# Kernel tuning notes

Measured on AMD Instinct MI355X. Metric: run time of the kernel, lower is better.

Reference implementation:

```python
import jax, jax.numpy as jnp
import numpy as np

DEPTH = 6; HEADS = 6; DIM = 384; HD = DIM // HEADS
WS = 14; WINDOW_BLOCKS = (0, 1, 3, 4)
IMG = 512; PATCH = 16; GRID = IMG // PATCH        # 32x32 token grid
PRE_GRID = 14                                      # 224 // 16 pretrain grid
SCALE = HD ** -0.5


def layer_norm(x, w, b, eps=1e-5):
    u = x.mean(-1, keepdims=True)
    s = ((x - u) ** 2).mean(-1, keepdims=True)
    return (x - u) / jnp.sqrt(s + eps) * w + b


def get_rel_pos(size, rel_pos):
    # q_size == k_size here; relative coords in [0, 2*size-2]
    coords = jnp.arange(size)[:, None] - jnp.arange(size)[None, :] + (size - 1)
    return rel_pos[coords]  # (size, size, HD)


def attention(x, qkv_w, qkv_b, proj_w, proj_b, rel_h, rel_w):
    B, H, W, C = x.shape
    N = H * W
    qkv = (x.reshape(B, N, C) @ qkv_w.T + qkv_b).reshape(B, N, 3, HEADS, HD)
    qkv = jnp.moveaxis(qkv, 2, 0).transpose(0, 1, 3, 2, 4)  # (3,B,h,N,d)
    q, k, v = qkv[0], qkv[1], qkv[2]
    attn = jnp.einsum('bhqd,bhkd->bhqk', q * SCALE, k)
    # decomposed relative position bias (ViTDet add_decomposed_rel_pos)
    Rh = get_rel_pos(H, rel_h)  # (H,H,d)
    Rw = get_rel_pos(W, rel_w)  # (W,W,d)
    rq = q.reshape(B, HEADS, H, W, HD)
    bias_h = jnp.einsum('bnhwc,hkc->bnhwk', rq, Rh)  # (B,h,H,W,H)
    bias_w = jnp.einsum('bnhwc,wkc->bnhwk', rq, Rw)  # (B,h,H,W,W)
    attn = (attn.reshape(B, HEADS, H, W, H, W)
            + bias_h[..., :, None] + bias_w[..., None, :]).reshape(B, HEADS, N, N)
    attn = jax.nn.softmax(attn, axis=-1)
    out = jnp.einsum('bhqk,bhkd->bhqd', attn, v)
    out = out.transpose(0, 2, 1, 3).reshape(B, H, W, C)
    return out @ proj_w.T + proj_b


def window_partition(x, ws):
    B, H, W, C = x.shape
    pad_h = (ws - H % ws) % ws
    pad_w = (ws - W % ws) % ws
    x = jnp.pad(x, ((0, 0), (0, pad_h), (0, pad_w), (0, 0)))
    Hp, Wp = H + pad_h, W + pad_w
    x = x.reshape(B, Hp // ws, ws, Wp // ws, ws, C)
    x = x.transpose(0, 1, 3, 2, 4, 5).reshape(-1, ws, ws, C)
    return x, Hp, Wp


def window_unpartition(win, ws, Hp, Wp, H, W):
    B = win.shape[0] // ((Hp // ws) * (Wp // ws))
    x = win.reshape(B, Hp // ws, Wp // ws, ws, ws, -1)
    x = x.transpose(0, 1, 3, 2, 4, 5).reshape(B, Hp, Wp, -1)
    return x[:, :H, :W]


def block(x, p, windowed):
    shortcut = x
    x = layer_norm(x, p['n1w'], p['n1b'])
    if windowed:
        H, W = x.shape[1], x.shape[2]
        x, Hp, Wp = window_partition(x, WS)
    x = attention(x, p['qw'], p['qb'], p['pw'], p['pb'], p['rh'], p['rw'])
    if windowed:
        x = window_unpartition(x, WS, Hp, Wp, H, W)
    x = shortcut + x
    h = layer_norm(x, p['n2w'], p['n2b'])
    h = jax.nn.gelu(h @ p['f1w'].T + p['f1b'], approximate=False)
    return x + h @ p['f2w'].T + p['f2b']


def vit_forward(x, patch_w, patch_b, pos_embed, norm1_w, norm1_b, qkv_w, qkv_b,
                proj_w, proj_b, norm2_w, norm2_b, fc1_w, fc1_b, fc2_w, fc2_b,
                rel_pos_h, rel_pos_w):
    y = jax.lax.conv_general_dilated(
        x, patch_w, (PATCH, PATCH), 'VALID',
        dimension_numbers=('NCHW', 'OIHW', 'NCHW'))
    y = y.transpose(0, 2, 3, 1) + patch_b  # (B, GRID, GRID, DIM)
    # abs pos embed: bicubic resize from pretrain 14x14 grid to 32x32
    pos = pos_embed.reshape(1, PRE_GRID, PRE_GRID, DIM)
    pos = jax.image.resize(pos, (1, GRID, GRID, DIM), 'bicubic')
    y = y + pos
    for i in range(DEPTH):
        windowed = i in WINDOW_BLOCKS
        L = 2 * WS - 1 if windowed else 2 * GRID - 1
        p = dict(n1w=norm1_w[i], n1b=norm1_b[i], qw=qkv_w[i], qb=qkv_b[i],
                 pw=proj_w[i], pb=proj_b[i], rh=rel_pos_h[i, :L], rw=rel_pos_w[i, :L],
                 n2w=norm2_w[i], n2b=norm2_b[i], f1w=fc1_w[i], f1b=fc1_b[i],
                 f2w=fc2_w[i], f2b=fc2_b[i])
        y = block(y, p, windowed)
    return y.transpose(0, 3, 1, 2)  # (B, DIM, GRID, GRID) 'last_feat'


def setup_inputs() -> dict:
    key = jax.random.key(0)
    ks = jax.random.split(key, 10)
    B = 4
    std = 0.02
    f32 = jnp.float32
    return {
        'x': jax.random.normal(ks[0], (B, 3, IMG, IMG), f32),
        'patch_w': jax.random.normal(ks[1], (DIM, 3, PATCH, PATCH), f32) * 0.05,
        'patch_b': jnp.zeros((DIM,), f32),
        'pos_embed': jax.random.normal(ks[2], (1, PRE_GRID * PRE_GRID, DIM), f32) * std,
        'norm1_w': jnp.ones((DEPTH, DIM), f32),
        'norm1_b': jnp.zeros((DEPTH, DIM), f32),
        'qkv_w': jax.random.normal(ks[3], (DEPTH, 3 * DIM, DIM), f32) * std,
        'qkv_b': jnp.zeros((DEPTH, 3 * DIM), f32),
        'proj_w': jax.random.normal(ks[4], (DEPTH, DIM, DIM), f32) * std,
        'proj_b': jnp.zeros((DEPTH, DIM), f32),
        'norm2_w': jnp.ones((DEPTH, DIM), f32),
        'norm2_b': jnp.zeros((DEPTH, DIM), f32),
        'fc1_w': jax.random.normal(ks[5], (DEPTH, 4 * DIM, DIM), f32) * std,
        'fc1_b': jnp.zeros((DEPTH, 4 * DIM), f32),
        'fc2_w': jax.random.normal(ks[6], (DEPTH, DIM, 4 * DIM), f32) * std,
        'fc2_b': jnp.zeros((DEPTH, DIM), f32),
        'rel_pos_h': jax.random.normal(ks[7], (DEPTH, 2 * GRID - 1, HD), f32) * std,
        'rel_pos_w': jax.random.normal(ks[8], (DEPTH, 2 * GRID - 1, HD), f32) * std,
    }


def reference(x, patch_w, patch_b, pos_embed, norm1_w, norm1_b, qkv_w, qkv_b,
              proj_w, proj_b, norm2_w, norm2_b, fc1_w, fc1_b, fc2_w, fc2_b,
              rel_pos_h, rel_pos_w):
    return vit_forward(x, patch_w, patch_b, pos_embed, norm1_w, norm1_b, qkv_w, qkv_b,
                       proj_w, proj_b, norm2_w, norm2_b, fc1_w, fc1_b, fc2_w, fc2_b,
                       rel_pos_h, rel_pos_w)
```

## Files before the change

### kernel.cpp

```cpp
#include <hip/hip_runtime.h>
#include <hip/hip_bf16.h>
#include <math.h>

#define B_SZ 4
#define DIM 384
#define HEADS 6
#define HD 64
#define NTOK 4096
#define WS 14
#define NWIN 36
#define WTOK 196

typedef unsigned short u16;
typedef __bf16 bf16_t;
typedef bf16_t bf16x8 __attribute__((ext_vector_type(8)));
typedef float f32x4 __attribute__((ext_vector_type(4)));

__device__ __forceinline__ float bf2f(unsigned u) { return __uint_as_float(u << 16); }
__device__ __forceinline__ u16 f2bf(float f) {
    unsigned u = __float_as_uint(f);
    unsigned r = (u + 0x7fffu + ((u >> 16) & 1u)) >> 16;
    return (u16)r;
}
__device__ __forceinline__ unsigned pk2bf(float a, float b) {
    __hip_bfloat162 h = __float22bfloat162_rn(make_float2(a, b));
    unsigned r; __builtin_memcpy(&r, &h, 4); return r;
}

__device__ __forceinline__ void ldsload16(const u16* g, u16* l) {
    __builtin_amdgcn_global_load_lds(
        (const __attribute__((address_space(1))) unsigned int*)g,
        (__attribute__((address_space(3))) unsigned int*)l, 16, 0, 0);
}

__device__ __forceinline__ int swz(int r) { return (r ^ (r >> 2)) & 3; }

__device__ inline float cubic_keys(float x) {
    x = fabsf(x);
    if (x <= 1.f) return ((1.5f * x - 2.5f) * x) * x + 1.f;
    if (x < 2.f)  return ((-0.5f * x + 2.5f) * x - 4.f) * x + 2.f;
    return 0.f;
}

__global__ __launch_bounds__(256) void setup_kernel(
        const float* __restrict__ p0, const float* __restrict__ p1,
        const float* __restrict__ p2, const float* __restrict__ p3,
        const float* __restrict__ p4, const float* __restrict__ p5,
        u16* __restrict__ wb, const float* __restrict__ pe,
        float* __restrict__ posr, const float* __restrict__ x,
        u16* __restrict__ col) {
    int i = (blockIdx.x * 256 + threadIdx.x) * 4;
    if (i < 10918656) {
        const float* s; int off;
        if      (i <   294912) { s = p0; off = 0; }
        else if (i <  2949120) { s = p1; off = 294912; }
        else if (i <  3833856) { s = p2; off = 2949120; }
        else if (i <  7372800) { s = p3; off = 3833856; }
        else if (i < 10911744) { s = p4; off = 7372800; }
        else                   { s = p5; off = 10911744; }
        float4 v = *(const float4*)(s + (i - off));
        u16 o[4] = { f2bf(v.x), f2bf(v.y), f2bf(v.z), f2bf(v.w) };
        *(uint2*)(wb + i) = *(const uint2*)o;
        return;
    }
    i -= 10918656;
    if (i < 393216) {
        int c = i % 384;
        int g = i / 384;
        int gy = g / 32, gx = g % 32;
        float wy[14], wx[14];
        float sy = (gy + 0.5f) * (14.f / 32.f) - 0.5f;
        float sx = (gx + 0.5f) * (14.f / 32.f) - 0.5f;
        float toty = 0.f, totx = 0.f;
        #pragma unroll
        for (int k = 0; k < 14; ++k) {
            wy[k] = cubic_keys(sy - (float)k); toty += wy[k];
            wx[k] = cubic_keys(sx - (float)k); totx += wx[k];
        }
        float4 acc = {0.f, 0.f, 0.f, 0.f};
        #pragma unroll 1
        for (int iy = 0; iy < 14; ++iy) {
            if (wy[iy] == 0.f) continue;
            float4 row = {0.f, 0.f, 0.f, 0.f};
            for (int ix = 0; ix < 14; ++ix) {
                if (wx[ix] == 0.f) continue;
                float4 pv = *(const float4*)(pe + (iy * 14 + ix) * 384 + c);
                row.x += wx[ix] * pv.x; row.y += wx[ix] * pv.y;
                row.z += wx[ix] * pv.z; row.w += wx[ix] * pv.w;
            }
            acc.x += wy[iy] * row.x; acc.y += wy[iy] * row.y;
            acc.z += wy[iy] * row.z; acc.w += wy[iy] * row.w;
        }
        float inv = 1.f / (toty * totx);
        acc.x *= inv; acc.y *= inv; acc.z *= inv; acc.w *= inv;
        *(float4*)(posr + i) = acc;
        return;
    }
    i -= 393216;
    if (i < 3145728) {
        int kk = i % 768;
        int p  = i / 768;
        int b  = p / 1024;
        int ph = (p % 1024) / 32;
        int pw = p % 32;
        int c = kk / 256;
        int r = kk % 256;
        int ii = r / 16, j = r % 16;
        float4 v = *(const float4*)(x + (size_t)b * 3 * 512 * 512 +
                                    (size_t)c * 512 * 512 +
                                    (size_t)(ph * 16 + ii) * 512 + (pw * 16 + j));
        u16 o[4] = { f2bf(v.x), f2bf(v.y), f2bf(v.z), f2bf(v.w) };
        *(uint2*)(col + i) = *(const uint2*)o;
    }
}

__global__ __launch_bounds__(64) void epi_ln_kernel(const float* __restrict__ P,
        const float* __restrict__ bias, const float* __restrict__ posr,
        float* __restrict__ y, int addy, int nsk,
        const float* __restrict__ lw, const float* __restrict__ lb,
        u16* __restrict__ lnout, float* __restrict__ outT)
{
    int tok = blockIdx.x, t = threadIdx.x;
    size_t base = (size_t)tok * 384;
    float v[6];
    float s = 0.f;
    #pragma unroll
    for (int i = 0; i < 6; ++i) {
        int c = t + 64 * i;
        float val = bias[c];
        #pragma unroll 1
        for (int sk = 0; sk < nsk; ++sk)
            val += P[(size_t)sk * 1572864 + base + c];
        if (posr) val += posr[(size_t)(tok & 1023) * 384 + c];
        if (addy) val += y[base + c];
        v[i] = val; s += val;
    }
    if (outT) {
        int b = tok >> 10, g = tok & 1023;
        #pragma unroll
        for (int i = 0; i < 6; ++i) {
            int c = t + 64 * i;
            outT[((size_t)(b * 384 + c)) * 1024 + g] = v[i];
        }
        return;
    }
    #pragma unroll
    for (int i = 0; i < 6; ++i) y[base + t + 64 * i] = v[i];
    if (!lnout) return;
    #pragma unroll
    for (int off = 32; off > 0; off >>= 1) s += __shfl_xor(s, off);
    float mean = s * (1.f / 384.f);
    float vs = 0.f;
    #pragma unroll
    for (int i = 0; i < 6; ++i) { float d = v[i] - mean; vs += d * d; }
    #pragma unroll
    for (int off = 32; off > 0; off >>= 1) vs += __shfl_xor(vs, off);
    float inv = rsqrtf(vs * (1.f / 384.f) + 1e-5f);
    u16* orow = lnout + base;
    #pragma unroll
    for (int i = 0; i < 6; ++i) {
        int c = t + 64 * i;
        orow[c] = f2bf((v[i] - mean) * inv * lw[c] + lb[c]);
    }
}

__global__ __launch_bounds__(256) void mfma_gemm4(
        const u16* __restrict__ A, const u16* __restrict__ Wt,
        const float* __restrict__ bias,
        float* __restrict__ outf, u16* __restrict__ outb,
        float* __restrict__ outp,
        int M, int N, int K, int act, int ksplit)
{
    __shared__ u16 As[2][8192];
    __shared__ u16 Bs[2][4096];
    int t = threadIdx.x;
    int lane = t & 63, wave = t >> 6;
    int wm = (wave >> 1) * 64, wn = (wave & 1) * 32;
    int m0 = blockIdx.y * 128, n0 = blockIdx.x * 64;
    int ks = blockIdx.z * ksplit;

    int r0 = t >> 2,        c0 = ((t & 3) ^ swz(t >> 2)) * 8;
    int r1 = 64 + (t >> 2), c1 = ((t & 3) ^ swz(64 + (t >> 2))) * 8;
    const u16* a0 = A + (size_t)(m0 + r0) * K + c0;
    const u16* a1 = A + (size_t)(m0 + r1) * K + c1;
    const u16* b0 = Wt + (size_t)(n0 + r0) * K + c0;

    auto stage = [&](int k0, int buf) {
        ldsload16(a0 + k0,      &As[buf][wave * 512]);
        ldsload16(a1 + k0,      &As[buf][2048 + wave * 512]);
        ldsload16(b0 + k0,      &Bs[buf][wave * 512]);
        ldsload16(a0 + k0 + 32, &As[buf][4096 + wave * 512]);
        ldsload16(a1 + k0 + 32, &As[buf][6144 + wave * 512]);
        ldsload16(b0 + k0 + 32, &Bs[buf][2048 + wave * 512]);
    };

    f32x4 acc[4][2] = {};
    int row_a = wm + (lane & 15);
    int row_b = wn + (lane & 15);
    int lq = lane >> 4;
    int nchunks = ksplit / 64;

    stage(ks, 0);
    __syncthreads();

    for (int ci = 0; ci < nchunks; ++ci) {
        int p = ci & 1;
        bool pref = (ci + 1 < nchunks);
        if (pref) stage(ks + (ci + 1) * 64, 1 - p);
        #pragma unroll
        for (int hf = 0; hf < 2; ++hf) {
            bf16x8 af[4], bfr[2];
            #pragma unroll
            for (int i = 0; i < 4; ++i) {
                int r = row_a + i * 16;
                af[i] = *(const bf16x8*)&As[p][hf * 4096 + r * 32 + ((lq ^ swz(r)) * 8)];
            }
            #pragma unroll
            for (int j = 0; j < 2; ++j) {
                int r = row_b + j * 16;
                bfr[j] = *(const bf16x8*)&Bs[p][hf * 2048 + r * 32 + ((lq ^ swz(r)) * 8)];
            }
            #pragma unroll
            for (int i = 0; i < 4; ++i)
                #pragma unroll
                for (int j = 0; j < 2; ++j)
                    acc[i][j] = __builtin_amdgcn_mfma_f32_16x16x32_bf16(
                        af[i], bfr[j], acc[i][j], 0, 0, 0);
        }
        if (pref) __syncthreads();
    }

    int colq = lane & 15, rowq = (lane >> 4) * 4;
    if (outp) {
        float* pp = outp + (size_t)blockIdx.z * M * N;
        #pragma unroll
        for (int i = 0; i < 4; ++i) {
            #pragma unroll
            for (int rr = 0; rr < 4; ++rr) {
                int m = m0 + wm + i * 16 + rowq + rr;
                size_t mo = (size_t)m * N;
                #pragma unroll
                for (int j = 0; j < 2; ++j) {
                    int n = n0 + wn + j * 16 + colq;
                    pp[mo + n] = acc[i][j][rr];
                }
            }
        }
        return;
    }
    #pragma unroll
    for (int i = 0; i < 4; ++i) {
        #pragma unroll
        for (int rr = 0; rr < 4; ++rr) {
            int m = m0 + wm + i * 16 + rowq + rr;
            size_t mo = (size_t)m * N;
            #pragma unroll
            for (int j = 0; j < 2; ++j) {
                int n = n0 + wn + j * 16 + colq;
                float v = acc[i][j][rr] + bias[n];
                if (act)  v = 0.5f * v * (1.f + erff(v * 0.70710678118654752f));
                if (outf) outf[mo + n] = v;
                if (outb) outb[mo + n] = f2bf(v);
            }
        }
    }
}

template<int N, int W>
__global__ __launch_bounds__(256) void attn_mfma(const u16* __restrict__ qkv,
        const u16* __restrict__ qkb, const float* __restrict__ rh,
        const float* __restrict__ rw, u16* __restrict__ outb,
        float* __restrict__ opart, float* __restrict__ lpart)
{
    constexpr int JS = (W == 32) ? 64 : 32;
    constexpr int L  = (W == 32) ? 63 : 27;
    constexpr int CTR = W - 1;
    constexpr int KSPAN = (W == 32) ? 512 : 224;
    constexpr int NKT = KSPAN / 32;
    __shared__ u16 KV[11776];
    __shared__ u16 bhl[64 * 66];
    __shared__ u16 bwl[64 * 66];
    __shared__ u16 Qt[64 * 66];

    u16* Pb = KV + 9216;
    u16* Rt = KV;

    int t = threadIdx.x, lane = t & 63, wave = t >> 6;
    int quad = lane >> 4, l15 = lane & 15;
    int uh = blockIdx.x, qb0 = blockIdx.y * 64;
    int z = (W == 32) ? blockIdx.z : 0;
    int kstart = z * KSPAN;
    int h = uh % HEADS, u = uh / HEADS;
    size_t tbase = (size_t)u * 1024;
    int wb_ = u / 9, wr = u - wb_ * 9;
    int wy = wr / 3, wx = wr - wy * 3;

    auto tok14 = [&](int iy, int ix) -> const u16* {
        int gy = wy * WS + iy, gx = wx * WS + ix;
        if (gy < 32 && gx < 32)
            return qkv + (size_t)(wb_ * 1024 + gy * 32 + gx) * 1152;
        return qkb;
    };
    auto rowptr = [&](int lq2) -> const u16* {
        if constexpr (W == 32) {
            return qkv + (tbase + lq2) * 1152;
        } else {
            int iy = lq2 / WS, ix = lq2 - iy * WS;
            return tok14(iy, ix);
        }
    };

    {
        int q = t & 63, ch0 = (t >> 6) * 16;
        int qc = qb0 + q; if (qc >= N) qc = N - 1;
        const u16* qp = rowptr(qc) + h * 64 + ch0;
        uint4 a = *(const uint4*)qp;
        uint4 b = *(const uint4*)(qp + 8);
        u16 vals[16];
        *(uint4*)vals = a; *(uint4*)(vals + 8) = b;
        #pragma unroll
        for (int c = 0; c < 16; ++c)
            Qt[(ch0 + c) * 66 + q] = ((qb0 + q) < N) ? vals[c] : (u16)0;
    }

    #pragma unroll
    for (int table = 0; table < 2; ++table) {
        __syncthreads();
        const float* tab = table ? rw : rh;
        for (int idx = t; idx < JS * 8; idx += 256) {
            int j = idx >> 3, cc0 = (idx & 7) * 8;
            u16 tmp[8];
            if (j < L) {
                const float* src = tab + (size_t)j * 64 + cc0;
                #pragma unroll
                for (int c = 0; c < 8; ++c) tmp[c] = f2bf(src[c]);
            } else {
                #pragma unroll
                for (int c = 0; c < 8; ++c) tmp[c] = 0;
            }
            *(uint4*)&Rt[j * 72 + cc0] = *(uint4*)tmp;
        }
        __syncthreads();
        if (wave < JS / 16) {
            int jt = wave;
            bf16x8 af0 = *(const bf16x8*)&Rt[(jt * 16 + l15) * 72 + quad * 8];
            bf16x8 af1 = *(const bf16x8*)&Rt[(jt * 16 + l15) * 72 + 32 + quad * 8];
            u16* dst = table ? bwl : bhl;
            #pragma unroll
            for (int qt = 0; qt < 4; ++qt) {
                bf16x8 qf0, qf1;
                u16* p0 = (u16*)&qf0; u16* p1 = (u16*)&qf1;
                #pragma unroll
                for (int zz = 0; zz < 8; ++zz) {
                    p0[zz] = Qt[(quad * 8 + zz) * 66 + qt * 16 + l15];
                    p1[zz] = Qt[(32 + quad * 8 + zz) * 66 + qt * 16 + l15];
                }
                f32x4 acc = {};
                acc = __builtin_amdgcn_mfma_f32_16x16x32_bf16(af0, qf0, acc, 0, 0, 0);
                acc = __builtin_amdgcn_mfma_f32_16x16x32_bf16(af1, qf1, acc, 0, 0, 0);
                #pragma unroll
                for (int r = 0; r < 4; ++r)
                    dst[(qt * 16 + l15) * 66 + jt * 16 + quad * 4 + r] = f2bf(acc[r]);
            }
        }
    }
    __syncthreads();

    int skey = (wave * 64 + lane) >> 3;
    int sc8  = ((wave * 64 + lane) & 7) ^ (skey & 7);
    int vkey = t & 31, vch0 = (t >> 5) * 8;
    int siy = 0, six = 0, viy = 0, vix = 0;
    if constexpr (W != 32) {
        int k0 = kstart + skey;
        siy = k0 / WS; six = k0 - siy * WS;
        int k1 = kstart + vkey;
        viy = k1 / WS; vix = k1 - viy * WS;
    }
    auto adv = [](int& iy, int& ix) { ix += 4; iy += 2; if (ix >= WS) { ix -= WS; ++iy; } };

    {
        const u16* kp = (W == 32) ? qkv + (tbase + kstart + skey) * 1152
                                  : tok14(siy, six);
        ldsload16(kp + 384 + h * 64 + sc8 * 8, KV + wave * 512);
        const u16* vp = (W == 32) ? qkv + (tbase + kstart + vkey) * 1152
                                  : tok14(viy, vix);
        uint4 vv = *(const uint4*)(vp + 768 + h * 64 + vch0);
        u16 tmp[8]; *(uint4*)tmp = vv;
        u16* vdst = KV + 4096;
        #pragma unroll
        for (int c = 0; c < 8; ++c) vdst[(vch0 + c) * 40 + vkey] = tmp[c];
        if constexpr (W != 32) { adv(siy, six); adv(viy, vix); }
    }

    bf16x8 qf[2];
    #pragma unroll
    for (int hc = 0; hc < 2; ++hc) {
        u16* qv = (u16*)&qf[hc];
        #pragma unroll
        for (int j = 0; j < 8; ++j)
            qv[j] = Qt[(hc * 32 + quad * 8 + j) * 66 + wave * 16 + l15];
    }
    int qme = wave * 16 + l15;
    int qq = qb0 + qme; if (qq >= N) qq = N - 1;
    int qh = qq / W, qw = qq - qh * W;
    float bwreg[2][4];
    int kh_[2][4], kw_[2][4];
    #pragma unroll
    for (int kc2 = 0; kc2 < 2; ++kc2)
        #pragma unroll
        for (int r = 0; r < 4; ++r) {
            int keyl = kc2 * 16 + quad * 4 + r;
            if constexpr (W == 32) {
                bwreg[kc2][r] = bf2f(bwl[qme * 66 + (qw - keyl + CTR)]);
            } else {
                kh_[kc2][r] = keyl / WS;
                kw_[kc2][r] = keyl - kh_[kc2][r] * WS;
            }
        }

    f32x4 of[4] = {};
    float lsum = 0.f;
    __syncthreads();

    for (int kt = 0; kt < NKT; ++kt) {
        int kb = kstart + kt * 32;
        int p = kt & 1;
        const u16* ksp = KV + p * 2048;
        const u16* vtp = KV + 4096 + p * 2560;
        bool pref = (kt + 1 < NKT);
        uint4 vpref;
        if (pref) {
            const u16* kp = (W == 32) ? qkv + (tbase + kb + 32 + skey) * 1152
                                      : tok14(siy, six);
            ldsload16(kp + 384 + h * 64 + sc8 * 8, KV + (1 - p) * 2048 + wave * 512);
            const u16* vp = (W == 32) ? qkv + (tbase + kb + 32 + vkey) * 1152
                                      : tok14(viy, vix);
            vpref = *(const uint4*)(vp + 768 + h * 64 + vch0);
            if constexpr (W != 32) { adv(siy, six); adv(viy, vix); }
        }

        f32x4 st[2] = {};
        #pragma unroll
        for (int hc = 0; hc < 2; ++hc) {
            #pragma unroll
            for (int kc2 = 0; kc2 < 2; ++kc2) {
                int key = kc2 * 16 + l15;
                int c8 = hc * 4 + quad;
                int pp = key * 8 + (c8 ^ (key & 7));
                bf16x8 kf = *(const bf16x8*)&ksp[pp * 8];
                st[kc2] = __builtin_amdgcn_mfma_f32_16x16x32_bf16(
                    kf, qf[hc], st[kc2], 0, 0, 0);
            }
        }
        float bh_t = 0.f;
        if constexpr (W == 32) bh_t = bf2f(bhl[qme * 66 + (qh - (kb >> 5) + CTR)]);
        #pragma unroll
        for (int kc2 = 0; kc2 < 2; ++kc2) {
            float pv4[4];
            #pragma unroll
            for (int r = 0; r < 4; ++r) {
                int keyl = kc2 * 16 + quad * 4 + r;
                float b;
                if constexpr (W == 32) {
                    b = bh_t + bwreg[kc2][r];
                } else {
                    b = bf2f(bhl[qme * 66 + (qh - kh_[kc2][r] + CTR)]) +
                        bf2f(bwl[qme * 66 + (qw - kw_[kc2][r] + CTR)]);
                }
                float pv = __expf(fmaf(st[kc2][r], 0.125f, b));
                if (kb + keyl >= N) pv = 0.f;
                lsum += pv;
                pv4[r] = pv;
            }
            uint2 pk;
            pk.x = pk2bf(pv4[0], pv4[1]);
            pk.y = pk2bf(pv4[2], pv4[3]);
            *(uint2*)&Pb[wave * 640 + l15 * 40 + kc2 * 16 + quad * 4] = pk;
        }
        if constexpr (W != 32) {
            #pragma unroll
            for (int kc2 = 0; kc2 < 2; ++kc2)
                #pragma unroll
                for (int r = 0; r < 4; ++r) {
                    kw_[kc2][r] += 4; kh_[kc2][r] += 2;
                    if (kw_[kc2][r] >= WS) { kw_[kc2][r] -= WS; ++kh_[kc2][r]; }
                }
        }
        bf16x8 pf = *(const bf16x8*)&Pb[wave * 640 + l15 * 40 + quad * 8];
        #pragma unroll
        for (int ca = 0; ca < 4; ++ca) {
            bf16x8 vf = *(const bf16x8*)&vtp[(ca * 16 + l15) * 40 + quad * 8];
            of[ca] = __builtin_amdgcn_mfma_f32_16x16x32_bf16(
                vf, pf, of[ca], 0, 0, 0);
        }

        if (pref) {
            u16 tmp[8]; *(uint4*)tmp = vpref;
            u16* vdst = KV + 4096 + (1 - p) * 2560;
            #pragma unroll
            for (int c = 0; c < 8; ++c) vdst[(vch0 + c) * 40 + vkey] = tmp[c];
            __syncthreads();
        }
    }

    lsum += __shfl_xor(lsum, 16);
    lsum += __shfl_xor(lsum, 32);
    int q = qb0 + qme;
    if constexpr (W == 32) {
        size_t ridx = (size_t)z * 24576 + (size_t)uh * 1024 + q;
        float* op = opart + ridx * 64;
        #pragma unroll
        for (int ca = 0; ca < 4; ++ca)
            *(float4*)&op[ca * 16 + quad * 4] = (float4){of[ca][0], of[ca][1],
                                                         of[ca][2], of[ca][3]};
        if (quad == 0) lpart[ridx] = lsum;
    } else {
        float inv = 1.f / lsum;
        if (q < N) {
            int iy = q / WS, ix = q - iy * WS;
            int gy = wy * WS + iy, gx = wx * WS + ix;
            if (gy >= 32 || gx >= 32) return;
            u16* op = outb + (size_t)(wb_ * 1024 + gy * 32 + gx) * 384 + h * 64;
            #pragma unroll
            for (int ca = 0; ca < 4; ++ca) {
                uint2 pk;
                pk.x = pk2bf(of[ca][0] * inv, of[ca][1] * inv);
                pk.y = pk2bf(of[ca][2] * inv, of[ca][3] * inv);
                *(uint2*)&op[ca * 16 + quad * 4] = pk;
            }
        }
    }
}

__global__ __launch_bounds__(256) void attn_merge_kernel(const float* __restrict__ O,
        const float* __restrict__ Lp, u16* __restrict__ attb)
{
    int t = threadIdx.x;
    int idx = blockIdx.x * 4 + (t >> 6);
    int ch = t & 63;
    float o = O[(size_t)idx * 64 + ch] + O[((size_t)24576 + idx) * 64 + ch];
    float l = Lp[idx] + Lp[24576 + idx];
    int uh = idx >> 10, q = idx & 1023;
    int u = uh / 6, h = uh - u * 6;
    attb[((size_t)(u * 1024 + q)) * 384 + h * 64 + ch] = f2bf(o / l);
}

static inline void launch_gemm(const u16* A, const u16* W, const float* bias,
                               float* outf, u16* outb,
                               int M, int N, int K, int act, hipStream_t s) {
    dim3 g(N / 64, M / 128, 1);
    mfma_gemm4<<<g, 256, 0, s>>>(A, W, bias, outf, outb, nullptr, M, N, K, act, K);
}

static inline void launch_gemm_sk(const u16* A, const u16* W, float* P,
                                  int M, int N, int K, int SK, hipStream_t s) {
    dim3 g(N / 64, M / 128, SK);
    mfma_gemm4<<<g, 256, 0, s>>>(A, W, nullptr, nullptr, nullptr, P,
                                 M, N, K, 0, K / SK);
}

extern "C" void kernel_launch(void* const* d_in, const int* in_sizes, int n_in,
                              void* d_out, int out_size, void* d_ws, size_t ws_size,
                              hipStream_t stream) {
    const float* x      = (const float*)d_in[0];
    const float* patchw = (const float*)d_in[1];
    const float* patchb = (const float*)d_in[2];
    const float* pos    = (const float*)d_in[3];
    const float* n1w    = (const float*)d_in[4];
    const float* n1b    = (const float*)d_in[5];
    const float* qkvw   = (const float*)d_in[6];
    const float* qkvb   = (const float*)d_in[7];
    const float* pw     = (const float*)d_in[8];
    const float* pb     = (const float*)d_in[9];
    const float* n2w    = (const float*)d_in[10];
    const float* n2b    = (const float*)d_in[11];
    const float* f1w    = (const float*)d_in[12];
    const float* f1b    = (const float*)d_in[13];
    const float* f2w    = (const float*)d_in[14];
    const float* f2b    = (const float*)d_in[15];
    const float* rph    = (const float*)d_in[16];
    const float* rpw    = (const float*)d_in[17];
    float* out = (float*)d_out;

    float* y   = (float*)d_ws;
    u16* attb  = (u16*)(y + 1572864);
    u16* mlpb  = attb + 1572864;
    u16* lnb   = mlpb + 6291456;
    u16* qkvx  = lnb + 1572864;
    u16* rsrv  = qkvx + 4718592;
    u16* wb    = rsrv + 7864320;
    float* posr = (float*)(wb + 10918656);

    u16* colb  = rsrv;
    float* P_patch = (float*)attb;
    float* P_pf    = (float*)qkvx;
    float* Opart   = (float*)mlpb;
    float* Lpart   = (float*)lnb;

    u16* wb_patch = wb;
    u16* wb_qkv   = wb + 294912;
    u16* wb_pw    = wb + 2949120;
    u16* wb_f1    = wb + 3833856;
    u16* wb_f2    = wb + 7372800;
    u16* wqb      = wb + 10911744;

    setup_kernel<<<(14457600 / 4 + 255) / 256, 256, 0, stream>>>(
        patchw, qkvw, pw, f1w, f2w, qkvb, wb, pos, posr, x, colb);

    launch_gemm_sk(colb, wb_patch, P_patch, NTOK, 384, 768, 2, stream);
    epi_ln_kernel<<<NTOK, 64, 0, stream>>>(P_patch, patchb, posr, y, 0, 2,
                                           n1w, n1b, lnb, nullptr);

    for (int i = 0; i < 6; ++i) {
        bool windowed = (i == 0 || i == 1 || i == 3 || i == 4);
        const float* rh = rph + (size_t)i * 63 * 64;
        const float* rw = rpw + (size_t)i * 63 * 64;
        launch_gemm(lnb, wb_qkv + (size_t)i * 442368, qkvb + i * 1152,
                    nullptr, qkvx, NTOK, 1152, 384, 0, stream);
        if (windowed) {
            attn_mfma<WTOK, WS><<<dim3(NWIN * HEADS, 4, 1), 256, 0, stream>>>(
                qkvx, wqb + i * 1152, rh, rw, attb, nullptr, nullptr);
        } else {
            attn_mfma<1024, 32><<<dim3(B_SZ * HEADS, 16, 2), 256, 0, stream>>>(
                qkvx, wqb + i * 1152, rh, rw, nullptr, Opart, Lpart);
            attn_merge_kernel<<<6144, 256, 0, stream>>>(Opart, Lpart, attb);
        }
        launch_gemm_sk(attb, wb_pw + (size_t)i * 147456, P_pf,
                       NTOK, 384, 384, 2, stream);
        epi_ln_kernel<<<NTOK, 64, 0, stream>>>(P_pf, pb + i * 384, nullptr, y, 1, 2,
                                               n2w + i * 384, n2b + i * 384, lnb,
                                               nullptr);
        launch_gemm(lnb, wb_f1 + (size_t)i * 589824, f1b + i * 1536,
                    nullptr, mlpb, NTOK, 1536, 384, 1, stream);
        launch_gemm_sk(mlpb, wb_f2 + (size_t)i * 589824, P_pf,
                       NTOK, 384, 1536, 2, stream);
        if (i < 5)
            epi_ln_kernel<<<NTOK, 64, 0, stream>>>(P_pf, f2b + i * 384, nullptr, y,
                                                   1, 2, n1w + (i + 1) * 384,
                                                   n1b + (i + 1) * 384, lnb, nullptr);
        else
            epi_ln_kernel<<<NTOK, 64, 0, stream>>>(P_pf, f2b + i * 384, nullptr, y,
                                                   1, 2, nullptr, nullptr, nullptr,
                                                   out);
    }
}
```

Baseline: 752.1 us.

## Accumulate split-K GEMM partials atomically into residual, slimmer LN and transpose kernels

The proj and fc2 split-K GEMMs now add bias and atomically accumulate their partial sums straight into the residual stream y, so the separate partial buffers and their reduction in the epilogue kernel go away. A lighter LayerNorm-only kernel with four tokens per block replaces the epilogue, and the final output goes through a tiled LDS transpose instead of strided scattered stores. Windowed attention waves whose 16 queries are all padding now skip their compute. The atomics make the summation order nondeterministic and add read-modify-write traffic on y.

```diff
diff --git a/kernel.cpp b/kernel.cpp
--- a/kernel.cpp
+++ b/kernel.cpp
@@ -118,7 +118,7 @@
         const float* __restrict__ bias, const float* __restrict__ posr,
         float* __restrict__ y, int addy, int nsk,
         const float* __restrict__ lw, const float* __restrict__ lb,
-        u16* __restrict__ lnout, float* __restrict__ outT)
+        u16* __restrict__ lnout)
 {
     int tok = blockIdx.x, t = threadIdx.x;
     size_t base = (size_t)tok * 384;
@@ -135,15 +135,6 @@
         if (addy) val += y[base + c];
         v[i] = val; s += val;
     }
-    if (outT) {
-        int b = tok >> 10, g = tok & 1023;
-        #pragma unroll
-        for (int i = 0; i < 6; ++i) {
-            int c = t + 64 * i;
-            outT[((size_t)(b * 384 + c)) * 1024 + g] = v[i];
-        }
-        return;
-    }
     #pragma unroll
     for (int i = 0; i < 6; ++i) y[base + t + 64 * i] = v[i];
     if (!lnout) return;
@@ -161,6 +152,58 @@
     for (int i = 0; i < 6; ++i) {
         int c = t + 64 * i;
         orow[c] = f2bf((v[i] - mean) * inv * lw[c] + lb[c]);
+    }
+}
+
+__global__ __launch_bounds__(256) void ln_kernel(const float* __restrict__ y,
+        const float* __restrict__ lw, const float* __restrict__ lb,
+        u16* __restrict__ lnout)
+{
+    int tok = blockIdx.x * 4 + (threadIdx.x >> 6);
+    int t = threadIdx.x & 63;
+    size_t base = (size_t)tok * 384;
+    float v[6];
+    float s = 0.f;
+    #pragma unroll
+    for (int i = 0; i < 6; ++i) {
+        v[i] = y[base + t + 64 * i]; s += v[i];
+    }
+    #pragma unroll
+    for (int off = 32; off > 0; off >>= 1) s += __shfl_xor(s, off);
+    float mean = s * (1.f / 384.f);
+    float vs = 0.f;
+    #pragma unroll
+    for (int i = 0; i < 6; ++i) { float d = v[i] - mean; vs += d * d; }
+    #pragma unroll
+    for (int off = 32; off > 0; off >>= 1) vs += __shfl_xor(vs, off);
+    float inv = rsqrtf(vs * (1.f / 384.f) + 1e-5f);
+    u16* orow = lnout + base;
+    #pragma unroll
+    for (int i = 0; i < 6; ++i) {
+        int c = t + 64 * i;
+        orow[c] = f2bf((v[i] - mean) * inv * lw[c] + lb[c]);
+    }
+}
+
+__global__ __launch_bounds__(256) void out_transpose(const float* __restrict__ y,
+        float* __restrict__ outT)
+{
+    __shared__ float T[64][65];
+    int c0 = blockIdx.x * 64, m0 = blockIdx.y * 64;
+    int t = threadIdx.x;
+    int cl = t & 63, wv = t >> 6;
+    #pragma unroll
+    for (int r = 0; r < 16; ++r) {
+        int ml = wv * 16 + r;
+        T[ml][cl] = y[(size_t)(m0 + ml) * 384 + c0 + cl];
+    }
+    __syncthreads();
+    int b = m0 >> 10, g0 = m0 & 1023;
+    int gl = t & 63;
+    #pragma unroll
+    for (int r = 0; r < 16; ++r) {
+        int ccl = wv * 16 + r;
+        outT[((size_t)(b * 384 + c0 + ccl)) * 1024 + g0 + gl] = T[gl][ccl];
     }
 }
 
@@ -169,7 +212,7 @@
         const float* __restrict__ bias,
         float* __restrict__ outf, u16* __restrict__ outb,
         float* __restrict__ outp,
-        int M, int N, int K, int act, int ksplit)
+        int M, int N, int K, int act, int ksplit, int atomicf)
 {
     __shared__ u16 As[2][8192];
     __shared__ u16 Bs[2][4096];
@@ -231,6 +274,24 @@
     }
 
     int colq = lane & 15, rowq = (lane >> 4) * 4;
+    if (atomicf) {
+        #pragma unroll
+        for (int i = 0; i < 4; ++i) {
+            #pragma unroll
+            for (int rr = 0; rr < 4; ++rr) {
+                int m = m0 + wm + i * 16 + rowq + rr;
+                size_t mo = (size_t)m * N;
+                #pragma unroll
+                for (int j = 0; j < 2; ++j) {
+                    int n = n0 + wn + j * 16 + colq;
+                    float v = acc[i][j][rr];
+                    if (blockIdx.z == 0) v += bias[n];
+                    unsafeAtomicAdd(outf + mo + n, v);
+                }
+            }
+        }
+        return;
+    }
     if (outp) {
         float* pp = outp + (size_t)blockIdx.z * M * N;
         #pragma unroll
@@ -401,6 +462,7 @@
             qv[j] = Qt[(hc * 32 + quad * 8 + j) * 66 + wave * 16 + l15];
     }
     int qme = wave * 16 + l15;
+    bool wactive = (W == 32) ? true : ((qb0 + wave * 16) < N);
     int qq = qb0 + qme; if (qq >= N) qq = N - 1;
     int qh = qq / W, qw = qq - qh * W;
     float bwreg[2][4];
@@ -439,59 +501,61 @@
             if constexpr (W != 32) { adv(siy, six); adv(viy, vix); }
         }
 
-        f32x4 st[2] = {};
-        #pragma unroll
-        for (int hc = 0; hc < 2; ++hc) {
+        if (wactive) {
+            f32x4 st[2] = {};
+            #pragma unroll
+            for (int hc = 0; hc < 2; ++hc) {
+                #pragma unroll
+                for (int kc2 = 0; kc2 < 2; ++kc2) {
+                    int key = kc2 * 16 + l15;
+                    int c8 = hc * 4 + quad;
+                    int pp = key * 8 + (c8 ^ (key & 7));
+                    bf16x8 kf = *(const bf16x8*)&ksp[pp * 8];
+                    st[kc2] = __builtin_amdgcn_mfma_f32_16x16x32_bf16(
+                        kf, qf[hc], st[kc2], 0, 0, 0);
+                }
+            }
+            float bh_t = 0.f;
+            if constexpr (W == 32) bh_t = bf2f(bhl[qme * 66 + (qh - (kb >> 5) + CTR)]);
             #pragma unroll
             for (int kc2 = 0; kc2 < 2; ++kc2) {
-                int key = kc2 * 16 + l15;
-                int c8 = hc * 4 + quad;
-                int pp = key * 8 + (c8 ^ (key & 7));
-                bf16x8 kf = *(const bf16x8*)&ksp[pp * 8];
-                st[kc2] = __builtin_amdgcn_mfma_f32_16x16x32_bf16(
-                    kf, qf[hc], st[kc2], 0, 0, 0);
-            }
-        }
-        float bh_t = 0.f;
-        if constexpr (W == 32) bh_t = bf2f(bhl[qme * 66 + (qh - (kb >> 5) + CTR)]);
-        #pragma unroll
-        for (int kc2 = 0; kc2 < 2; ++kc2) {
-            float pv4[4];
-            #pragma unroll
-            for (int r = 0; r < 4; ++r) {
-                int keyl = kc2 * 16 + quad * 4 + r;
-                float b;
-                if constexpr (W == 32) {
-                    b = bh_t + bwreg[kc2][r];
-                } else {
-                    b = bf2f(bhl[qme * 66 + (qh - kh_[kc2][r] + CTR)]) +
-                        bf2f(bwl[qme * 66 + (qw - kw_[kc2][r] + CTR)]);
+                float pv4[4];
+                #pragma unroll
+                for (int r = 0; r < 4; ++r) {
+                    int keyl = kc2 * 16 + quad * 4 + r;
+                    float b;
+                    if constexpr (W == 32) {
+                        b = bh_t + bwreg[kc2][r];
+                    } else {
+                        b = bf2f(bhl[qme * 66 + (qh - kh_[kc2][r] + CTR)]) +
+                            bf2f(bwl[qme * 66 + (qw - kw_[kc2][r] + CTR)]);
+                    }
+                    float pv = __expf(fmaf(st[kc2][r], 0.125f, b));
+                    if (kb + keyl >= N) pv = 0.f;
+                    lsum += pv;
+                    pv4[r] = pv;
                 }
-                float pv = __expf(fmaf(st[kc2][r], 0.125f, b));
-                if (kb + keyl >= N) pv = 0.f;
-                lsum += pv;
-                pv4[r] = pv;
-            }
-            uint2 pk;
-            pk.x = pk2bf(pv4[0], pv4[1]);
-            pk.y = pk2bf(pv4[2], pv4[3]);
-            *(uint2*)&Pb[wave * 640 + l15 * 40 + kc2 * 16 + quad * 4] = pk;
-        }
-        if constexpr (W != 32) {
-            #pragma unroll
-            for (int kc2 = 0; kc2 < 2; ++kc2)
-                #pragma unroll
-                for (int r = 0; r < 4; ++r) {
-                    kw_[kc2][r] += 4; kh_[kc2][r] += 2;
-                    if (kw_[kc2][r] >= WS) { kw_[kc2][r] -= WS; ++kh_[kc2][r]; }
-                }
-        }
-        bf16x8 pf = *(const bf16x8*)&Pb[wave * 640 + l15 * 40 + quad * 8];
-        #pragma unroll
-        for (int ca = 0; ca < 4; ++ca) {
-            bf16x8 vf = *(const bf16x8*)&vtp[(ca * 16 + l15) * 40 + quad * 8];
-            of[ca] = __builtin_amdgcn_mfma_f32_16x16x32_bf16(
-                vf, pf, of[ca], 0, 0, 0);
+                uint2 pk;
+                pk.x = pk2bf(pv4[0], pv4[1]);
+                pk.y = pk2bf(pv4[2], pv4[3]);
+                *(uint2*)&Pb[wave * 640 + l15 * 40 + kc2 * 16 + quad * 4] = pk;
+            }
+            if constexpr (W != 32) {
+                #pragma unroll
+                for (int kc2 = 0; kc2 < 2; ++kc2)
+                    #pragma unroll
+                    for (int r = 0; r < 4; ++r) {
+                        kw_[kc2][r] += 4; kh_[kc2][r] += 2;
+                        if (kw_[kc2][r] >= WS) { kw_[kc2][r] -= WS; ++kh_[kc2][r]; }
+                    }
+            }
+            bf16x8 pf = *(const bf16x8*)&Pb[wave * 640 + l15 * 40 + quad * 8];
+            #pragma unroll
+            for (int ca = 0; ca < 4; ++ca) {
+                bf16x8 vf = *(const bf16x8*)&vtp[(ca * 16 + l15) * 40 + quad * 8];
+                of[ca] = __builtin_amdgcn_mfma_f32_16x16x32_bf16(
+                    vf, pf, of[ca], 0, 0, 0);
+            }
         }
 
         if (pref) {
@@ -549,14 +613,22 @@
                                float* outf, u16* outb,
                                int M, int N, int K, int act, hipStream_t s) {
     dim3 g(N / 64, M / 128, 1);
-    mfma_gemm4<<<g, 256, 0, s>>>(A, W, bias, outf, outb, nullptr, M, N, K, act, K);
+    mfma_gemm4<<<g, 256, 0, s>>>(A, W, bias, outf, outb, nullptr, M, N, K, act, K, 0);
 }
 
 static inline void launch_gemm_sk(const u16* A, const u16* W, float* P,
                                   int M, int N, int K, int SK, hipStream_t s) {
     dim3 g(N / 64, M / 128, SK);
     mfma_gemm4<<<g, 256, 0, s>>>(A, W, nullptr, nullptr, nullptr, P,
-                                 M, N, K, 0, K / SK);
+                                 M, N, K, 0, K / SK, 0);
+}
+
+static inline void launch_gemm_at(const u16* A, const u16* W, const float* bias,
+                                  float* y, int M, int N, int K, int SK,
+                                  hipStream_t s) {
+    dim3 g(N / 64, M / 128, SK);
+    mfma_gemm4<<<g, 256, 0, s>>>(A, W, bias, y, nullptr, nullptr,
+                                 M, N, K, 0, K / SK, 1);
 }
 
 extern "C" void kernel_launch(void* const* d_in, const int* in_sizes, int n_in,
@@ -593,7 +665,6 @@
 
     u16* colb  = rsrv;
     float* P_patch = (float*)attb;
-    float* P_pf    = (float*)qkvx;
     float* Opart   = (float*)mlpb;
     float* Lpart   = (float*)lnb;
 
@@ -609,7 +680,7 @@
 
     launch_gemm_sk(colb, wb_patch, P_patch, NTOK, 384, 768, 2, stream);
     epi_ln_kernel<<<NTOK, 64, 0, stream>>>(P_patch, patchb, posr, y, 0, 2,
-                                           n1w, n1b, lnb, nullptr);
+                                           n1w, n1b, lnb);
 
     for (int i = 0; i < 6; ++i) {
         bool windowed = (i == 0 || i == 1 || i == 3 || i == 4);
@@ -625,22 +696,17 @@
                 qkvx, wqb + i * 1152, rh, rw, nullptr, Opart, Lpart);
             attn_merge_kernel<<<6144, 256, 0, stream>>>(Opart, Lpart, attb);
         }
-        launch_gemm_sk(attb, wb_pw + (size_t)i * 147456, P_pf,
+        launch_gemm_at(attb, wb_pw + (size_t)i * 147456, pb + i * 384, y,
                        NTOK, 384, 384, 2, stream);
-        epi_ln_kernel<<<NTOK, 64, 0, stream>>>(P_pf, pb + i * 384, nullptr, y, 1, 2,
-                                               n2w + i * 384, n2b + i * 384, lnb,
-                                               nullptr);
+        ln_kernel<<<1024, 256, 0, stream>>>(y, n2w + i * 384, n2b + i * 384, lnb);
         launch_gemm(lnb, wb_f1 + (size_t)i * 589824, f1b + i * 1536,
                     nullptr, mlpb, NTOK, 1536, 384, 1, stream);
-        launch_gemm_sk(mlpb, wb_f2 + (size_t)i * 589824, P_pf,
+        launch_gemm_at(mlpb, wb_f2 + (size_t)i * 589824, f2b + i * 384, y,
                        NTOK, 384, 1536, 2, stream);
         if (i < 5)
-            epi_ln_kernel<<<NTOK, 64, 0, stream>>>(P_pf, f2b + i * 384, nullptr, y,
-                                                   1, 2, n1w + (i + 1) * 384,
-                                                   n1b + (i + 1) * 384, lnb, nullptr);
+            ln_kernel<<<1024, 256, 0, stream>>>(y, n1w + (i + 1) * 384,
+                                                n1b + (i + 1) * 384, lnb);
         else
-            epi_ln_kernel<<<NTOK, 64, 0, stream>>>(P_pf, f2b + i * 384, nullptr, y,
-                                                   1, 2, nullptr, nullptr, nullptr,
-                                                   out);
-    }
-}
+            out_transpose<<<dim3(6, 64), 256, 0, stream>>>(y, out);
+    }
+}
```

Result: slower. 813.0 us (+8.1%).
